# Kernel optimization log

Hardware: AMD Instinct MI355X
Metric: run time of the kernel (lower is better)

## Reference

```python
import jax, jax.numpy as jnp
import numpy as np

D_MODEL = 1024
NHEAD = 16
HEAD_DIM = D_MODEL // NHEAD
SCALE = HEAD_DIM ** (-0.5)


def setup_inputs() -> dict:
    key = jax.random.key(0)
    k1, k2, k3 = jax.random.split(key, 3)
    B, T, C = 2, 2048, D_MODEL
    x = jax.random.normal(k1, (B, T, C), dtype=jnp.float32)
    W_qkv = jax.random.normal(k2, (3 * C, C), dtype=jnp.float32) * (C ** -0.5)
    b_qkv = jnp.zeros((3 * C,), dtype=jnp.float32)
    W_out = jax.random.normal(k3, (C, C), dtype=jnp.float32) * (C ** -0.5)
    b_out = jnp.zeros((C,), dtype=jnp.float32)
    return {"x": x, "W_qkv": W_qkv, "b_qkv": b_qkv, "W_out": W_out, "b_out": b_out}


def reference(x, W_qkv, b_qkv, W_out, b_out):
    B, T, C = x.shape
    H, hd = NHEAD, HEAD_DIM
    qkv = x @ W_qkv.T + b_qkv
    qkv = qkv.reshape(B, T, 3, H, hd).transpose(2, 0, 3, 1, 4)
    q, k, v = qkv[0], qkv[1], qkv[2]
    # scaled dot-product scores: (B,H,T,T)
    attn = jnp.einsum('bhqd,bhkd->bhqk', q, k) * SCALE
    # causal mask (is_causal=True): lower-triangular allowed
    causal = jnp.tril(jnp.ones((T, T), dtype=bool))
    attn = jnp.where(causal[None, None, :, :], attn, -jnp.inf)
    attn = jax.nn.softmax(attn, axis=-1)
    # (B,H,T,hd) -> (B,T,C)
    out = jnp.einsum('bhqk,bhkd->bhqd', attn, v)
    out = out.transpose(0, 2, 1, 3).reshape(B, T, C)
    out = out @ W_out.T + b_out
    return out
```

## Files before the change

### kernel.cpp

```cpp
#include <hip/hip_runtime.h>
#include <hip/hip_bf16.h>
#include <stdint.h>

#define D_MODEL 1024
#define NHEAD   16
#define HEAD_DIM 64
#define BATCH   2
#define SEQ     2048
#define M_TOK   (BATCH*SEQ)
#define N_QKV   (3*D_MODEL)
#define KDIM    1024
#define Q_SCALE (0.125f * 1.44269504088896f)

typedef __bf16 bf16_t;
typedef bf16_t bf16x8 __attribute__((ext_vector_type(8)));
typedef bf16_t bf16x4 __attribute__((ext_vector_type(4)));
typedef float  f32x4  __attribute__((ext_vector_type(4)));

__device__ __forceinline__ void gl_lds16(const void* g, void* l) {
    __builtin_amdgcn_global_load_lds(
        (__attribute__((address_space(1))) void*)(void*)(const_cast<void*>(g)),
        (__attribute__((address_space(3))) void*)l, 16, 0, 0);
}

#define N4_X  (M_TOK * KDIM / 4)
#define N4_W1 (N_QKV * KDIM / 4)
#define N4_W2 (D_MODEL * KDIM / 4)
__global__ void convert_all(const float* __restrict__ x,
                            const float* __restrict__ w1,
                            const float* __restrict__ w2,
                            bf16_t* __restrict__ ox,
                            bf16_t* __restrict__ o1,
                            bf16_t* __restrict__ o2) {
    int t = blockIdx.x * blockDim.x + threadIdx.x;
    const float* src;
    bf16_t* dst;
    int off;
    if (t < N4_X)                { src = x;  dst = ox; off = t; }
    else if (t < N4_X + N4_W1)   { src = w1; dst = o1; off = t - N4_X; }
    else                         { src = w2; dst = o2; off = t - N4_X - N4_W1; }
    float4 v = reinterpret_cast<const float4*>(src)[off];
    bf16x4 o = { (bf16_t)v.x, (bf16_t)v.y, (bf16_t)v.z, (bf16_t)v.w };
    reinterpret_cast<bf16x4*>(dst)[off] = o;
}

template <int MODE>
__global__ __launch_bounds__(256) void gemm_bt(
    const bf16_t* __restrict__ A,
    const bf16_t* __restrict__ Bw,
    const float*  __restrict__ bias,
    int N,
    bf16_t* __restrict__ qkv_out,
    bf16_t* __restrict__ vt_out,
    float*  __restrict__ f32_out)
{
    __shared__ bf16_t As[128 * 64];
    __shared__ bf16_t Bs[128 * 64];

    const int cpx = gridDim.x >> 3;
    const int bid = (blockIdx.x & 7) * cpx + (blockIdx.x >> 3);

    const int nbn = N / 128;
    const int bm = bid / nbn;
    const int bn = bid % nbn;
    const int m0 = bm * 128, n0 = bn * 128;
    const int tid = threadIdx.x, wave = tid >> 6, lane = tid & 63;
    const int wr = wave >> 1, wc = wave & 1;

    f32x4 acc[4][4] = {};

    const int srow = lane >> 3;
    const int scol = ((lane & 7) ^ srow) * 8;
    const bf16_t* gA0 = A  + (size_t)(m0 + wave * 32 + srow) * KDIM + scol;
    const bf16_t* gB0 = Bw + (size_t)(n0 + wave * 32 + srow) * KDIM + scol;
    bf16_t* lA0 = &As[(wave * 32) * 64];
    bf16_t* lB0 = &Bs[(wave * 32) * 64];

    const int fr = lane & 15;
    const int kq = lane >> 4;

    for (int k0 = 0; k0 < KDIM; k0 += 64) {
#pragma unroll
        for (int c = 0; c < 4; c++) {
            gl_lds16(gA0 + (size_t)(c * 8) * KDIM + k0, lA0 + (c * 8) * 64);
            gl_lds16(gB0 + (size_t)(c * 8) * KDIM + k0, lB0 + (c * 8) * 64);
        }
        __syncthreads();

        bf16x8 af[2][4], bfr[2][4];
#pragma unroll
        for (int kk = 0; kk < 2; kk++) {
            const int ch = (((kk << 2) | kq) ^ (fr & 7)) * 8;
#pragma unroll
            for (int i = 0; i < 4; i++)
                af[kk][i] = *reinterpret_cast<const bf16x8*>(
                    &As[(wr * 64 + i * 16 + fr) * 64 + ch]);
#pragma unroll
            for (int j = 0; j < 4; j++)
                bfr[kk][j] = *reinterpret_cast<const bf16x8*>(
                    &Bs[(wc * 64 + j * 16 + fr) * 64 + ch]);
        }
        __builtin_amdgcn_s_setprio(1);
#pragma unroll
        for (int i = 0; i < 4; i++)
#pragma unroll
            for (int j = 0; j < 4; j++) {
                acc[i][j] = __builtin_amdgcn_mfma_f32_16x16x32_bf16(
                    af[0][i], bfr[0][j], acc[i][j], 0, 0, 0);
                acc[i][j] = __builtin_amdgcn_mfma_f32_16x16x32_bf16(
                    af[1][i], bfr[1][j], acc[i][j], 0, 0, 0);
            }
        __builtin_amdgcn_s_setprio(0);
        __syncthreads();
    }

#pragma unroll
    for (int i = 0; i < 4; i++) {
#pragma unroll
        for (int j = 0; j < 4; j++) {
            const int col = n0 + wc * 64 + j * 16 + fr;
            const float bv = bias[col];
            const int row0 = m0 + wr * 64 + i * 16 + kq * 4;
            if (MODE == 1) {
#pragma unroll
                for (int r = 0; r < 4; r++)
                    f32_out[(size_t)(row0 + r) * N + col] = acc[i][j][r] + bv;
            } else if (col < 1024) {
#pragma unroll
                for (int r = 0; r < 4; r++)
                    qkv_out[(size_t)(row0 + r) * N_QKV + col] =
                        (bf16_t)((acc[i][j][r] + bv) * Q_SCALE);
            } else if (col < 2048) {
#pragma unroll
                for (int r = 0; r < 4; r++)
                    qkv_out[(size_t)(row0 + r) * N_QKV + col] =
                        (bf16_t)(acc[i][j][r] + bv);
            } else {
                const int d = col & 63, hh = (col >> 6) & 15;
                const int bb = row0 >> 11, t0 = row0 & 2047;
                bf16x4 pv = { (bf16_t)(acc[i][j][0] + bv),
                              (bf16_t)(acc[i][j][1] + bv),
                              (bf16_t)(acc[i][j][2] + bv),
                              (bf16_t)(acc[i][j][3] + bv) };
                *reinterpret_cast<bf16x4*>(
                    &vt_out[((size_t)((bb * NHEAD + hh) * HEAD_DIM + d)) * SEQ + t0]) = pv;
            }
        }
    }
}

__global__ __launch_bounds__(512) void attn_fwd(
    const bf16_t* __restrict__ qkv,
    const bf16_t* __restrict__ Vt,
    bf16_t* __restrict__ O)
{
    __shared__ bf16_t Ks[2][64 * 64];
    __shared__ bf16_t Vs[2][64 * 64];
    __shared__ bf16_t Ps[8][32 * 72];

    const int nq2 = SEQ / 128;
    const int nbh = BATCH * NHEAD;
    const int qt2 = (nq2 - 1) - (blockIdx.x / nbh);
    const int bh = blockIdx.x % nbh;
    const int b = bh >> 4, h = bh & 15;
    const int q0 = qt2 * 128;
    const int tid = threadIdx.x, wave = tid >> 6, lane = tid & 63;
    const int group = wave >> 2;
    const int w4 = wave & 3;
    const int fr = lane & 15;
    const int kq = lane >> 4;
    const int sw = fr & 7;
    const int c0 = (kq ^ sw) * 8;
    const int c1 = ((kq + 4) ^ sw) * 8;

    bf16x8 qf0[2], qf1[2];
    {
        const int cbase = h * 64 + kq * 8;
        const size_t r0 = (size_t)(b * SEQ + q0 + w4 * 32 + fr);
        const size_t r1 = r0 + 16;
        qf0[0] = *reinterpret_cast<const bf16x8*>(&qkv[r0 * N_QKV + cbase]);
        qf0[1] = *reinterpret_cast<const bf16x8*>(&qkv[r0 * N_QKV + cbase + 32]);
        qf1[0] = *reinterpret_cast<const bf16x8*>(&qkv[r1 * N_QKV + cbase]);
        qf1[1] = *reinterpret_cast<const bf16x8*>(&qkv[r1 * N_QKV + cbase + 32]);
    }

    f32x4 acc0[4] = {}, acc1[4] = {};
    float l0 = 0.f, l1 = 0.f;

    const int srow = lane >> 3;
    const int scol = ((lane & 7) ^ srow) * 8;
    const bf16_t* gK = qkv + (size_t)(b * SEQ) * N_QKV + (D_MODEL + h * 64);
    const bf16_t* gV = Vt + (size_t)(bh * 64) * SEQ;

    const int ntpg = qt2 + 1;
    const int base_t = group * ntpg;

    for (int it = 0; it < ntpg; ++it) {
        const int g_it = base_t + it;
        const int kv0 = g_it * 64;
#pragma unroll
        for (int c = 0; c < 2; c++) {
            const int row = c * 32 + w4 * 8 + srow;
            gl_lds16(gK + (size_t)(kv0 + row) * N_QKV + scol,
                     &Ks[group][(c * 32 + w4 * 8) * 64]);
            gl_lds16(gV + (size_t)row * SEQ + kv0 + scol,
                     &Vs[group][(c * 32 + w4 * 8) * 64]);
        }
        __syncthreads();

        f32x4 s0[4], s1[4];
        __builtin_amdgcn_s_setprio(1);
#pragma unroll
        for (int j = 0; j < 4; j++) {
            bf16x8 k0f = *reinterpret_cast<const bf16x8*>(
                &Ks[group][(j * 16 + fr) * 64 + c0]);
            bf16x8 k1f = *reinterpret_cast<const bf16x8*>(
                &Ks[group][(j * 16 + fr) * 64 + c1]);
            f32x4 t = {0.f, 0.f, 0.f, 0.f};
            t = __builtin_amdgcn_mfma_f32_16x16x32_bf16(k0f, qf0[0], t, 0, 0, 0);
            t = __builtin_amdgcn_mfma_f32_16x16x32_bf16(k1f, qf0[1], t, 0, 0, 0);
            s0[j] = t;
            f32x4 u = {0.f, 0.f, 0.f, 0.f};
            u = __builtin_amdgcn_mfma_f32_16x16x32_bf16(k0f, qf1[0], u, 0, 0, 0);
            u = __builtin_amdgcn_mfma_f32_16x16x32_bf16(k1f, qf1[1], u, 0, 0, 0);
            s1[j] = u;
        }
        __builtin_amdgcn_s_setprio(0);

        if (g_it >= 2 * qt2) {
            const int qg0 = q0 + w4 * 32 + fr;
            const int qg1 = qg0 + 16;
#pragma unroll
            for (int j = 0; j < 4; j++)
#pragma unroll
                for (int r = 0; r < 4; r++) {
                    const int kvg = kv0 + j * 16 + kq * 4 + r;
                    if (kvg > qg0) s0[j][r] = -1e30f;
                    if (kvg > qg1) s1[j][r] = -1e30f;
                }
        }

        float rs0 = 0.f, rs1 = 0.f;
#pragma unroll
        for (int j = 0; j < 4; j++)
#pragma unroll
            for (int r = 0; r < 4; r++) {
                const float p0 = exp2f(s0[j][r]);
                const float p1 = exp2f(s1[j][r]);
                s0[j][r] = p0;
                s1[j][r] = p1;
                rs0 += p0;
                rs1 += p1;
            }
        l0 += rs0;
        l1 += rs1;

#pragma unroll
        for (int j = 0; j < 4; j++) {
            bf16x4 p0 = { (bf16_t)s0[j][0], (bf16_t)s0[j][1],
                          (bf16_t)s0[j][2], (bf16_t)s0[j][3] };
            *reinterpret_cast<bf16x4*>(&Ps[wave][fr * 72 + j * 16 + kq * 4]) = p0;
            bf16x4 p1 = { (bf16_t)s1[j][0], (bf16_t)s1[j][1],
                          (bf16_t)s1[j][2], (bf16_t)s1[j][3] };
            *reinterpret_cast<bf16x4*>(&Ps[wave][(16 + fr) * 72 + j * 16 + kq * 4]) = p1;
        }
        bf16x8 pa0 = *reinterpret_cast<const bf16x8*>(
            &Ps[wave][fr * 72 + kq * 8]);
        bf16x8 pa1 = *reinterpret_cast<const bf16x8*>(
            &Ps[wave][fr * 72 + 32 + kq * 8]);
        bf16x8 pb0 = *reinterpret_cast<const bf16x8*>(
            &Ps[wave][(16 + fr) * 72 + kq * 8]);
        bf16x8 pb1 = *reinterpret_cast<const bf16x8*>(
            &Ps[wave][(16 + fr) * 72 + 32 + kq * 8]);

        __builtin_amdgcn_s_setprio(1);
#pragma unroll
        for (int j = 0; j < 4; j++) {
            bf16x8 v0f = *reinterpret_cast<const bf16x8*>(
                &Vs[group][(j * 16 + fr) * 64 + c0]);
            bf16x8 v1f = *reinterpret_cast<const bf16x8*>(
                &Vs[group][(j * 16 + fr) * 64 + c1]);
            acc0[j] = __builtin_amdgcn_mfma_f32_16x16x32_bf16(v0f, pa0, acc0[j], 0, 0, 0);
            acc0[j] = __builtin_amdgcn_mfma_f32_16x16x32_bf16(v1f, pa1, acc0[j], 0, 0, 0);
            acc1[j] = __builtin_amdgcn_mfma_f32_16x16x32_bf16(v0f, pb0, acc1[j], 0, 0, 0);
            acc1[j] = __builtin_amdgcn_mfma_f32_16x16x32_bf16(v1f, pb1, acc1[j], 0, 0, 0);
        }
        __builtin_amdgcn_s_setprio(0);

        __syncthreads();
    }

    float* Cf = reinterpret_cast<float*>(&Ps[0][0]);
    const int pbase = w4 * 2176;
    if (group == 1) {
#pragma unroll
        for (int j = 0; j < 4; j++)
#pragma unroll
            for (int r = 0; r < 4; r++) {
                Cf[pbase + (j * 4 + r) * 64 + lane] = acc0[j][r];
                Cf[pbase + 1088 + (j * 4 + r) * 64 + lane] = acc1[j][r];
            }
        Cf[pbase + 1024 + lane] = l0;
        Cf[pbase + 1088 + 1024 + lane] = l1;
    }
    __syncthreads();
    if (group == 0) {
#pragma unroll
        for (int j = 0; j < 4; j++)
#pragma unroll
            for (int r = 0; r < 4; r++) {
                acc0[j][r] += Cf[pbase + (j * 4 + r) * 64 + lane];
                acc1[j][r] += Cf[pbase + 1088 + (j * 4 + r) * 64 + lane];
            }
        l0 += Cf[pbase + 1024 + lane];
        l1 += Cf[pbase + 1088 + 1024 + lane];

        l0 += __shfl_xor(l0, 16);
        l0 += __shfl_xor(l0, 32);
        l1 += __shfl_xor(l1, 16);
        l1 += __shfl_xor(l1, 32);
        const float inv0 = 1.0f / l0;
        const float inv1 = 1.0f / l1;
        const size_t row0 = (size_t)(b * SEQ + q0 + w4 * 32 + fr);
        const size_t row1 = row0 + 16;
#pragma unroll
        for (int j = 0; j < 4; j++) {
            bf16x4 o0 = { (bf16_t)(acc0[j][0] * inv0), (bf16_t)(acc0[j][1] * inv0),
                          (bf16_t)(acc0[j][2] * inv0), (bf16_t)(acc0[j][3] * inv0) };
            *reinterpret_cast<bf16x4*>(&O[row0 * D_MODEL + h * 64 + j * 16 + kq * 4]) = o0;
            bf16x4 o1 = { (bf16_t)(acc1[j][0] * inv1), (bf16_t)(acc1[j][1] * inv1),
                          (bf16_t)(acc1[j][2] * inv1), (bf16_t)(acc1[j][3] * inv1) };
            *reinterpret_cast<bf16x4*>(&O[row1 * D_MODEL + h * 64 + j * 16 + kq * 4]) = o1;
        }
    }
}

extern "C" void kernel_launch(void* const* d_in, const int* in_sizes, int n_in,
                              void* d_out, int out_size, void* d_ws, size_t ws_size,
                              hipStream_t stream) {
    (void)in_sizes; (void)n_in; (void)out_size; (void)ws_size;
    const float* x    = (const float*)d_in[0];
    const float* Wqkv = (const float*)d_in[1];
    const float* bqkv = (const float*)d_in[2];
    const float* Wout = (const float*)d_in[3];
    const float* bout = (const float*)d_in[4];
    float* out = (float*)d_out;

    char* ws = (char*)d_ws;
    size_t off = 0;
    bf16_t* x_bf    = (bf16_t*)(ws + off); off += (size_t)M_TOK * KDIM * 2;
    bf16_t* wqkv_bf = (bf16_t*)(ws + off); off += (size_t)N_QKV * KDIM * 2;
    bf16_t* wout_bf = (bf16_t*)(ws + off); off += (size_t)D_MODEL * KDIM * 2;
    bf16_t* qkv     = (bf16_t*)(ws + off); off += (size_t)M_TOK * N_QKV * 2;
    bf16_t* vt      = (bf16_t*)(ws + off); off += (size_t)BATCH * NHEAD * HEAD_DIM * SEQ * 2;
    bf16_t* o_bf    = (bf16_t*)(ws + off); off += (size_t)M_TOK * D_MODEL * 2;

    convert_all<<<(N4_X + N4_W1 + N4_W2) / 256, 256, 0, stream>>>(
        x, Wqkv, Wout, x_bf, wqkv_bf, wout_bf);

    gemm_bt<0><<<(M_TOK / 128) * (N_QKV / 128), 256, 0, stream>>>(
        x_bf, wqkv_bf, bqkv, N_QKV, qkv, vt, nullptr);

    attn_fwd<<<(SEQ / 128) * BATCH * NHEAD, 512, 0, stream>>>(qkv, vt, o_bf);

    gemm_bt<1><<<(M_TOK / 128) * (D_MODEL / 128), 256, 0, stream>>>(
        o_bf, wout_bf, bout, D_MODEL, nullptr, nullptr, out);
}
```

Before: 108.7 us.

## Split attention KV loop across three wave groups with 768-thread blocks

The attention kernel now runs 12 waves in three groups instead of 8 waves in two, splitting the causal KV tiles three ways and reducing the partial accumulators of two groups into group 0 at the end. The P staging buffer is halved per wave by processing the two 16-row query halves one after another, reusing the buffer, so LDS fits in a single raw allocation of about 75 KB. This aims to shorten the per-block serial KV loop and raise parallelism. In exchange, some groups idle on uneven splits, the shared barrier count is unchanged, LDS use is larger, and the bigger blocks may lower occupancy.

```diff
diff --git a/kernel.cpp b/kernel.cpp
--- a/kernel.cpp
+++ b/kernel.cpp
@@ -149,14 +149,16 @@
     }
 }
 
-__global__ __launch_bounds__(512) void attn_fwd(
+__global__ __launch_bounds__(768) void attn_fwd(
     const bf16_t* __restrict__ qkv,
     const bf16_t* __restrict__ Vt,
     bf16_t* __restrict__ O)
 {
-    __shared__ bf16_t Ks[2][64 * 64];
-    __shared__ bf16_t Vs[2][64 * 64];
-    __shared__ bf16_t Ps[8][32 * 72];
+    __shared__ __align__(16) char smem_raw[76800];
+    bf16_t* Ks = (bf16_t*)smem_raw;
+    bf16_t* Vs = (bf16_t*)(smem_raw + 24576);
+    bf16_t* Ps = (bf16_t*)(smem_raw + 49152);
+    float*  Cf = (float*)smem_raw;
 
     const int nq2 = SEQ / 128;
     const int nbh = BATCH * NHEAD;
@@ -173,6 +175,10 @@
     const int c0 = (kq ^ sw) * 8;
     const int c1 = ((kq + 4) ^ sw) * 8;
 
+    bf16_t* myK = Ks + group * 4096;
+    bf16_t* myV = Vs + group * 4096;
+    bf16_t* myP = Ps + wave * (16 * 72);
+
     bf16x8 qf0[2], qf1[2];
     {
         const int cbase = h * 64 + kq * 8;
@@ -192,128 +198,151 @@
     const bf16_t* gK = qkv + (size_t)(b * SEQ) * N_QKV + (D_MODEL + h * 64);
     const bf16_t* gV = Vt + (size_t)(bh * 64) * SEQ;
 
-    const int ntpg = qt2 + 1;
-    const int base_t = group * ntpg;
-
-    for (int it = 0; it < ntpg; ++it) {
-        const int g_it = base_t + it;
+    const int nt = 2 * qt2 + 2;
+    const int q3 = nt / 3, rem = nt % 3;
+    const int cnt = q3 + (group < rem ? 1 : 0);
+    const int base = group * q3 + (group < rem ? group : rem);
+    const int iters = q3 + (rem ? 1 : 0);
+
+    for (int it = 0; it < iters; ++it) {
+        const bool act = (it < cnt);
+        const int g_it = base + it;
         const int kv0 = g_it * 64;
-#pragma unroll
-        for (int c = 0; c < 2; c++) {
-            const int row = c * 32 + w4 * 8 + srow;
-            gl_lds16(gK + (size_t)(kv0 + row) * N_QKV + scol,
-                     &Ks[group][(c * 32 + w4 * 8) * 64]);
-            gl_lds16(gV + (size_t)row * SEQ + kv0 + scol,
-                     &Vs[group][(c * 32 + w4 * 8) * 64]);
+        if (act) {
+#pragma unroll
+            for (int c = 0; c < 2; c++) {
+                const int row = w4 * 16 + c * 8 + srow;
+                gl_lds16(gK + (size_t)(kv0 + row) * N_QKV + scol,
+                         myK + (w4 * 16 + c * 8) * 64);
+                gl_lds16(gV + (size_t)row * SEQ + kv0 + scol,
+                         myV + (w4 * 16 + c * 8) * 64);
+            }
         }
         __syncthreads();
 
-        f32x4 s0[4], s1[4];
-        __builtin_amdgcn_s_setprio(1);
-#pragma unroll
-        for (int j = 0; j < 4; j++) {
-            bf16x8 k0f = *reinterpret_cast<const bf16x8*>(
-                &Ks[group][(j * 16 + fr) * 64 + c0]);
-            bf16x8 k1f = *reinterpret_cast<const bf16x8*>(
-                &Ks[group][(j * 16 + fr) * 64 + c1]);
-            f32x4 t = {0.f, 0.f, 0.f, 0.f};
-            t = __builtin_amdgcn_mfma_f32_16x16x32_bf16(k0f, qf0[0], t, 0, 0, 0);
-            t = __builtin_amdgcn_mfma_f32_16x16x32_bf16(k1f, qf0[1], t, 0, 0, 0);
-            s0[j] = t;
-            f32x4 u = {0.f, 0.f, 0.f, 0.f};
-            u = __builtin_amdgcn_mfma_f32_16x16x32_bf16(k0f, qf1[0], u, 0, 0, 0);
-            u = __builtin_amdgcn_mfma_f32_16x16x32_bf16(k1f, qf1[1], u, 0, 0, 0);
-            s1[j] = u;
-        }
-        __builtin_amdgcn_s_setprio(0);
-
-        if (g_it >= 2 * qt2) {
-            const int qg0 = q0 + w4 * 32 + fr;
-            const int qg1 = qg0 + 16;
+        if (act) {
+            f32x4 s0[4], s1[4];
+            __builtin_amdgcn_s_setprio(1);
+#pragma unroll
+            for (int j = 0; j < 4; j++) {
+                bf16x8 k0f = *reinterpret_cast<const bf16x8*>(
+                    &myK[(j * 16 + fr) * 64 + c0]);
+                bf16x8 k1f = *reinterpret_cast<const bf16x8*>(
+                    &myK[(j * 16 + fr) * 64 + c1]);
+                f32x4 t = {0.f, 0.f, 0.f, 0.f};
+                t = __builtin_amdgcn_mfma_f32_16x16x32_bf16(k0f, qf0[0], t, 0, 0, 0);
+                t = __builtin_amdgcn_mfma_f32_16x16x32_bf16(k1f, qf0[1], t, 0, 0, 0);
+                s0[j] = t;
+                f32x4 u = {0.f, 0.f, 0.f, 0.f};
+                u = __builtin_amdgcn_mfma_f32_16x16x32_bf16(k0f, qf1[0], u, 0, 0, 0);
+                u = __builtin_amdgcn_mfma_f32_16x16x32_bf16(k1f, qf1[1], u, 0, 0, 0);
+                s1[j] = u;
+            }
+            __builtin_amdgcn_s_setprio(0);
+
+            if (g_it >= 2 * qt2) {
+                const int qg0 = q0 + w4 * 32 + fr;
+                const int qg1 = qg0 + 16;
+#pragma unroll
+                for (int j = 0; j < 4; j++)
+#pragma unroll
+                    for (int r = 0; r < 4; r++) {
+                        const int kvg = kv0 + j * 16 + kq * 4 + r;
+                        if (kvg > qg0) s0[j][r] = -1e30f;
+                        if (kvg > qg1) s1[j][r] = -1e30f;
+                    }
+            }
+
+            float rs0 = 0.f, rs1 = 0.f;
 #pragma unroll
             for (int j = 0; j < 4; j++)
 #pragma unroll
                 for (int r = 0; r < 4; r++) {
-                    const int kvg = kv0 + j * 16 + kq * 4 + r;
-                    if (kvg > qg0) s0[j][r] = -1e30f;
-                    if (kvg > qg1) s1[j][r] = -1e30f;
+                    const float p0 = exp2f(s0[j][r]);
+                    const float p1 = exp2f(s1[j][r]);
+                    s0[j][r] = p0;
+                    s1[j][r] = p1;
+                    rs0 += p0;
+                    rs1 += p1;
                 }
-        }
-
-        float rs0 = 0.f, rs1 = 0.f;
+            l0 += rs0;
+            l1 += rs1;
+
+#pragma unroll
+            for (int j = 0; j < 4; j++) {
+                bf16x4 pq = { (bf16_t)s0[j][0], (bf16_t)s0[j][1],
+                              (bf16_t)s0[j][2], (bf16_t)s0[j][3] };
+                *reinterpret_cast<bf16x4*>(&myP[fr * 72 + j * 16 + kq * 4]) = pq;
+            }
+            {
+                bf16x8 pa0 = *reinterpret_cast<const bf16x8*>(&myP[fr * 72 + kq * 8]);
+                bf16x8 pa1 = *reinterpret_cast<const bf16x8*>(&myP[fr * 72 + 32 + kq * 8]);
+                __builtin_amdgcn_s_setprio(1);
+#pragma unroll
+                for (int j = 0; j < 4; j++) {
+                    bf16x8 v0f = *reinterpret_cast<const bf16x8*>(
+                        &myV[(j * 16 + fr) * 64 + c0]);
+                    bf16x8 v1f = *reinterpret_cast<const bf16x8*>(
+                        &myV[(j * 16 + fr) * 64 + c1]);
+                    acc0[j] = __builtin_amdgcn_mfma_f32_16x16x32_bf16(v0f, pa0, acc0[j], 0, 0, 0);
+                    acc0[j] = __builtin_amdgcn_mfma_f32_16x16x32_bf16(v1f, pa1, acc0[j], 0, 0, 0);
+                }
+                __builtin_amdgcn_s_setprio(0);
+            }
+
+#pragma unroll
+            for (int j = 0; j < 4; j++) {
+                bf16x4 pq = { (bf16_t)s1[j][0], (bf16_t)s1[j][1],
+                              (bf16_t)s1[j][2], (bf16_t)s1[j][3] };
+                *reinterpret_cast<bf16x4*>(&myP[fr * 72 + j * 16 + kq * 4]) = pq;
+            }
+            {
+                bf16x8 pb0 = *reinterpret_cast<const bf16x8*>(&myP[fr * 72 + kq * 8]);
+                bf16x8 pb1 = *reinterpret_cast<const bf16x8*>(&myP[fr * 72 + 32 + kq * 8]);
+                __builtin_amdgcn_s_setprio(1);
+#pragma unroll
+                for (int j = 0; j < 4; j++) {
+                    bf16x8 v0f = *reinterpret_cast<const bf16x8*>(
+                        &myV[(j * 16 + fr) * 64 + c0]);
+                    bf16x8 v1f = *reinterpret_cast<const bf16x8*>(
+                        &myV[(j * 16 + fr) * 64 + c1]);
+                    acc1[j] = __builtin_amdgcn_mfma_f32_16x16x32_bf16(v0f, pb0, acc1[j], 0, 0, 0);
+                    acc1[j] = __builtin_amdgcn_mfma_f32_16x16x32_bf16(v1f, pb1, acc1[j], 0, 0, 0);
+                }
+                __builtin_amdgcn_s_setprio(0);
+            }
+        }
+
+        __syncthreads();
+    }
+
+    if (group >= 1) {
+        const int cb = ((group - 1) * 4 + w4) * 2176;
 #pragma unroll
         for (int j = 0; j < 4; j++)
 #pragma unroll
             for (int r = 0; r < 4; r++) {
-                const float p0 = exp2f(s0[j][r]);
-                const float p1 = exp2f(s1[j][r]);
-                s0[j][r] = p0;
-                s1[j][r] = p1;
-                rs0 += p0;
-                rs1 += p1;
-            }
-        l0 += rs0;
-        l1 += rs1;
-
-#pragma unroll
-        for (int j = 0; j < 4; j++) {
-            bf16x4 p0 = { (bf16_t)s0[j][0], (bf16_t)s0[j][1],
-                          (bf16_t)s0[j][2], (bf16_t)s0[j][3] };
-            *reinterpret_cast<bf16x4*>(&Ps[wave][fr * 72 + j * 16 + kq * 4]) = p0;
-            bf16x4 p1 = { (bf16_t)s1[j][0], (bf16_t)s1[j][1],
-                          (bf16_t)s1[j][2], (bf16_t)s1[j][3] };
-            *reinterpret_cast<bf16x4*>(&Ps[wave][(16 + fr) * 72 + j * 16 + kq * 4]) = p1;
-        }
-        bf16x8 pa0 = *reinterpret_cast<const bf16x8*>(
-            &Ps[wave][fr * 72 + kq * 8]);
-        bf16x8 pa1 = *reinterpret_cast<const bf16x8*>(
-            &Ps[wave][fr * 72 + 32 + kq * 8]);
-        bf16x8 pb0 = *reinterpret_cast<const bf16x8*>(
-            &Ps[wave][(16 + fr) * 72 + kq * 8]);
-        bf16x8 pb1 = *reinterpret_cast<const bf16x8*>(
-            &Ps[wave][(16 + fr) * 72 + 32 + kq * 8]);
-
-        __builtin_amdgcn_s_setprio(1);
-#pragma unroll
-        for (int j = 0; j < 4; j++) {
-            bf16x8 v0f = *reinterpret_cast<const bf16x8*>(
-                &Vs[group][(j * 16 + fr) * 64 + c0]);
-            bf16x8 v1f = *reinterpret_cast<const bf16x8*>(
-                &Vs[group][(j * 16 + fr) * 64 + c1]);
-            acc0[j] = __builtin_amdgcn_mfma_f32_16x16x32_bf16(v0f, pa0, acc0[j], 0, 0, 0);
-            acc0[j] = __builtin_amdgcn_mfma_f32_16x16x32_bf16(v1f, pa1, acc0[j], 0, 0, 0);
-            acc1[j] = __builtin_amdgcn_mfma_f32_16x16x32_bf16(v0f, pb0, acc1[j], 0, 0, 0);
-            acc1[j] = __builtin_amdgcn_mfma_f32_16x16x32_bf16(v1f, pb1, acc1[j], 0, 0, 0);
-        }
-        __builtin_amdgcn_s_setprio(0);
-
-        __syncthreads();
-    }
-
-    float* Cf = reinterpret_cast<float*>(&Ps[0][0]);
-    const int pbase = w4 * 2176;
-    if (group == 1) {
-#pragma unroll
-        for (int j = 0; j < 4; j++)
-#pragma unroll
-            for (int r = 0; r < 4; r++) {
-                Cf[pbase + (j * 4 + r) * 64 + lane] = acc0[j][r];
-                Cf[pbase + 1088 + (j * 4 + r) * 64 + lane] = acc1[j][r];
-            }
-        Cf[pbase + 1024 + lane] = l0;
-        Cf[pbase + 1088 + 1024 + lane] = l1;
+                Cf[cb + (j * 4 + r) * 64 + lane] = acc0[j][r];
+                Cf[cb + 1088 + (j * 4 + r) * 64 + lane] = acc1[j][r];
+            }
+        Cf[cb + 1024 + lane] = l0;
+        Cf[cb + 1088 + 1024 + lane] = l1;
     }
     __syncthreads();
     if (group == 0) {
 #pragma unroll
-        for (int j = 0; j < 4; j++)
-#pragma unroll
-            for (int r = 0; r < 4; r++) {
-                acc0[j][r] += Cf[pbase + (j * 4 + r) * 64 + lane];
-                acc1[j][r] += Cf[pbase + 1088 + (j * 4 + r) * 64 + lane];
-            }
-        l0 += Cf[pbase + 1024 + lane];
-        l1 += Cf[pbase + 1088 + 1024 + lane];
+        for (int s = 0; s < 2; s++) {
+            const int cb = (s * 4 + w4) * 2176;
+#pragma unroll
+            for (int j = 0; j < 4; j++)
+#pragma unroll
+                for (int r = 0; r < 4; r++) {
+                    acc0[j][r] += Cf[cb + (j * 4 + r) * 64 + lane];
+                    acc1[j][r] += Cf[cb + 1088 + (j * 4 + r) * 64 + lane];
+                }
+            l0 += Cf[cb + 1024 + lane];
+            l1 += Cf[cb + 1088 + 1024 + lane];
+        }
 
         l0 += __shfl_xor(l0, 16);
         l0 += __shfl_xor(l0, 32);
@@ -361,7 +390,7 @@
     gemm_bt<0><<<(M_TOK / 128) * (N_QKV / 128), 256, 0, stream>>>(
         x_bf, wqkv_bf, bqkv, N_QKV, qkv, vt, nullptr);
 
-    attn_fwd<<<(SEQ / 128) * BATCH * NHEAD, 512, 0, stream>>>(qkv, vt, o_bf);
+    attn_fwd<<<(SEQ / 128) * BATCH * NHEAD, 768, 0, stream>>>(qkv, vt, o_bf);
 
     gemm_bt<1><<<(M_TOK / 128) * (D_MODEL / 128), 256, 0, stream>>>(
         o_bf, wout_bf, bout, D_MODEL, nullptr, nullptr, out);
```

Result: no change. 109.9 us (+1.1%).
